# Kernel tuning notes

Measured on AMD Instinct MI355X. Metric: run time of the kernel, lower is better.

Reference implementation:

```python
import jax, jax.numpy as jnp
import numpy as np

DIM = 64
NUM_GRAPHS = 512


def setup_inputs() -> dict:
    key = jax.random.key(0)
    ks = jax.random.split(key, 24)
    N, E, F = 20000, 60000, 11
    rn = lambda k, s, sc: jax.random.normal(k, s, jnp.float32) * sc
    return {
        "x": jax.random.normal(ks[0], (N, F), jnp.float32),
        "edge_index": jax.random.randint(ks[1], (2, E), 0, N),
        "edge_attr": jax.random.uniform(ks[2], (E, 5), jnp.float32),
        "batch": jnp.sort(jax.random.randint(ks[3], (N,), 0, NUM_GRAPHS)),
        # lin0: num_features -> dim
        "lin0_w": rn(ks[4], (DIM, F), 0.3), "lin0_b": jnp.zeros(DIM, jnp.float32),
        # edge MLP: 5 -> 128 -> dim*dim
        "nn1_w": rn(ks[5], (128, 5), 0.3), "nn1_b": jnp.zeros(128, jnp.float32),
        "nn2_w": rn(ks[6], (DIM * DIM, 128), 0.02), "nn2_b": jnp.zeros(DIM * DIM, jnp.float32),
        # NNConv root weight + bias
        "root_w": rn(ks[7], (DIM, DIM), 0.1), "conv_b": jnp.zeros(DIM, jnp.float32),
        # GRU (input dim, hidden dim) gates r,z,n
        "gru_w_ih": rn(ks[8], (3 * DIM, DIM), 0.1), "gru_w_hh": rn(ks[9], (3 * DIM, DIM), 0.1),
        "gru_b_ih": jnp.zeros(3 * DIM, jnp.float32), "gru_b_hh": jnp.zeros(3 * DIM, jnp.float32),
        # Set2Set LSTM: input 2*dim, hidden dim, gates i,f,g,o
        "lstm_w_ih": rn(ks[10], (4 * DIM, 2 * DIM), 0.1), "lstm_w_hh": rn(ks[11], (4 * DIM, DIM), 0.1),
        "lstm_b_ih": jnp.zeros(4 * DIM, jnp.float32), "lstm_b_hh": jnp.zeros(4 * DIM, jnp.float32),
        # readout
        "lin1_w": rn(ks[12], (DIM, 2 * DIM), 0.1), "lin1_b": jnp.zeros(DIM, jnp.float32),
        "lin2_w": rn(ks[13], (1, DIM), 0.1), "lin2_b": jnp.zeros(1, jnp.float32),
    }


def reference(x, edge_index, edge_attr, batch,
              lin0_w, lin0_b, nn1_w, nn1_b, nn2_w, nn2_b, root_w, conv_b,
              gru_w_ih, gru_w_hh, gru_b_ih, gru_b_hh,
              lstm_w_ih, lstm_w_hh, lstm_b_ih, lstm_b_hh,
              lin1_w, lin1_b, lin2_w, lin2_b):
    N = x.shape[0]
    src, dst = edge_index[0], edge_index[1]
    # per-edge weight matrices from edge MLP (edge_attr is constant across the 3 conv calls)
    We = (jax.nn.relu(edge_attr @ nn1_w.T + nn1_b) @ nn2_w.T + nn2_b).reshape(-1, DIM, DIM)
    deg = jnp.maximum(jax.ops.segment_sum(jnp.ones_like(src, jnp.float32), dst, N), 1.0)[:, None]

    out = jax.nn.relu(x @ lin0_w.T + lin0_b)
    h = out  # GRU hidden, shape [N, dim]
    for _ in range(3):
        # NNConv: gather src -> per-edge matmul -> scatter-mean at dst, plus root + bias
        msg = jnp.einsum('ei,eio->eo', out[src], We)
        agg = jax.ops.segment_sum(msg, dst, N) / deg
        m = jax.nn.relu(agg + out @ root_w.T + conv_b)
        # single GRU step (PyTorch gate layout r,z,n)
        gi = m @ gru_w_ih.T + gru_b_ih
        gh = h @ gru_w_hh.T + gru_b_hh
        ir, iz, inn = jnp.split(gi, 3, -1)
        hr, hz, hn = jnp.split(gh, 3, -1)
        r = jax.nn.sigmoid(ir + hr)
        z = jax.nn.sigmoid(iz + hz)
        n = jnp.tanh(inn + r * hn)
        h = (1.0 - z) * n + z * h
        out = h

    # Set2Set pooling, 3 processing steps
    B = NUM_GRAPHS
    q_star = jnp.zeros((B, 2 * DIM), out.dtype)
    hs = jnp.zeros((B, DIM), out.dtype)
    cs = jnp.zeros((B, DIM), out.dtype)
    for _ in range(3):
        gates = q_star @ lstm_w_ih.T + lstm_b_ih + hs @ lstm_w_hh.T + lstm_b_hh
        gi, gf, gg, go = jnp.split(gates, 4, -1)
        cs = jax.nn.sigmoid(gf) * cs + jax.nn.sigmoid(gi) * jnp.tanh(gg)
        hs = jax.nn.sigmoid(go) * jnp.tanh(cs)
        q = hs
        e = jnp.sum(out * q[batch], axis=-1)                 # [N]
        emax = jax.ops.segment_max(e, batch, B)
        a = jnp.exp(e - emax[batch])
        a = a / jax.ops.segment_sum(a, batch, B)[batch]      # scatter-softmax
        r_ = jax.ops.segment_sum(a[:, None] * out, batch, B)  # [B, dim]
        q_star = jnp.concatenate([q, r_], axis=-1)

    y = jax.nn.relu(q_star @ lin1_w.T + lin1_b) @ lin2_w.T + lin2_b
    return y.reshape(-1)
```

## Files before the change

### kernel.cpp

```cpp
#include <hip/hip_runtime.h>
#include <math.h>


typedef _Float16 f16x8 __attribute__((ext_vector_type(8)));
typedef _Float16 h2 __attribute__((ext_vector_type(2)));
typedef float f32x4 __attribute__((ext_vector_type(4)));

#define BFRAG_TOTAL (66 * 4 * 4 * 64 * 8)
#define GFRAG_TOTAL (4 * 16 * 64 * 8)
#define PAIRS_CAP 40064
#define PMAX 152
#define SPLITK 4
#define ITERS 8

#if __has_builtin(__builtin_amdgcn_fdot2)
#define FDOT2(a, b, c) __builtin_amdgcn_fdot2((a), (b), (c), false)
#else
__device__ __forceinline__ float FDOT2(h2 a, h2 b, float c) {
  return c + (float)a[0] * (float)b[0] + (float)a[1] * (float)b[1];
}
#endif

__global__ void k_gptr(const int* __restrict__ batch, int* __restrict__ gptr,
                       int N, int B) {
  int n = blockIdx.x * 256 + threadIdx.x;
  if (n >= N) return;
  int b = batch[n];
  int bp = (n == 0) ? -1 : batch[n - 1];
  for (int g = bp + 1; g <= b; ++g) gptr[g] = n;
  if (n == N - 1) {
    for (int g = b + 1; g <= B; ++g) gptr[g] = N;
  }
}

__global__ void k_cnt(const int* __restrict__ eidx, int* __restrict__ cnt, int E) {
  int e = blockIdx.x * 256 + threadIdx.x;
  if (e < E) atomicAdd(&cnt[eidx[E + e]], 1);
}

__global__ __launch_bounds__(1024) void k_scan(const int* __restrict__ cnt,
                                               int* __restrict__ dptr2, int N) {
  __shared__ int wsum[16];
  int t = threadIdx.x;
  int lane = t & 63, wid = t >> 6;
  if (t == 0) dptr2[0] = 0;
  int running = 0;
  for (int base = 0; base < N; base += 1024) {
    int x = (base + t < N) ? ((cnt[base + t] + 1) & ~1) : 0;
#pragma unroll
    for (int d = 1; d < 64; d <<= 1) {
      int u = __shfl_up(x, d, 64);
      if (lane >= d) x += u;
    }
    if (lane == 63) wsum[wid] = x;
    __syncthreads();
    if (wid == 0) {
      int y = (lane < 16) ? wsum[lane] : 0;
#pragma unroll
      for (int d = 1; d < 16; d <<= 1) {
        int u = __shfl_up(y, d, 64);
        if (lane >= d) y += u;
      }
      if (lane < 16) wsum[lane] = y;
    }
    __syncthreads();
    int add = running + (wid > 0 ? wsum[wid - 1] : 0);
    if (base + t < N) dptr2[base + t + 1] = add + x;
    running += wsum[15];
    __syncthreads();
  }
}

__global__ void k_fill(const int* __restrict__ eidx, const int* __restrict__ dptr2,
                       int* __restrict__ fill, int* __restrict__ srcs_s,
                       int* __restrict__ eord, int E) {
  int e = blockIdx.x * 256 + threadIdx.x;
  if (e >= E) return;
  int d = eidx[E + e];
  int pos = dptr2[d] + atomicAdd(&fill[d], 1);
  srcs_s[pos] = eidx[e];
  eord[pos] = e;
}

__global__ __launch_bounds__(256) void k_h1t(const float* __restrict__ eattr,
                                             const int* __restrict__ eord,
                                             const int* __restrict__ eidx,
                                             const int* __restrict__ cnt,
                                             const float* __restrict__ nn1_w,
                                             const float* __restrict__ nn1_b,
                                             f16x8* __restrict__ hp, int E) {
  __shared__ float w5[640];
  __shared__ float bb[128];
  __shared__ float at[128][10];
  __shared__ float idg[128];
  __shared__ float vf1[128];
  const int t = threadIdx.x;
  const int m0 = blockIdx.x * 128;
  for (int idx = t; idx < 640; idx += 256) w5[idx] = nn1_w[idx];
  if (t < 128) bb[t] = nn1_b[t];
  if (t < 128) {
    int m = m0 + t;
    int e0 = eord[2 * m], e1 = eord[2 * m + 1];
    float iv = 0.f, vf = 0.f;
    if (e0 >= 0) {
      const float* a = eattr + (size_t)e0 * 5;
#pragma unroll
      for (int q = 0; q < 5; ++q) at[t][q] = a[q];
      int dg = cnt[eidx[E + e0]];
      iv = 1.f / (float)(dg > 1 ? dg : 1);
      if (e1 >= 0) {
        const float* b = eattr + (size_t)e1 * 5;
#pragma unroll
        for (int q = 0; q < 5; ++q) at[t][5 + q] = b[q];
        vf = 1.f;
      } else {
#pragma unroll
        for (int q = 0; q < 5; ++q) at[t][5 + q] = 0.f;
      }
    } else {
#pragma unroll
      for (int q = 0; q < 10; ++q) at[t][q] = 0.f;
    }
    idg[t] = iv;
    vf1[t] = vf;
  }
  __syncthreads();
  const int pl = t & 127, jh = (t >> 7) * 64;
  const int m = m0 + pl;
  float a0 = at[pl][0], a1 = at[pl][1], a2 = at[pl][2], a3 = at[pl][3],
        a4 = at[pl][4];
  float b0 = at[pl][5], b1 = at[pl][6], b2 = at[pl][7], b3 = at[pl][8],
        b4 = at[pl][9];
  float iv = idg[pl], vf = vf1[pl];
#pragma unroll 4
  for (int ci = 0; ci < 16; ++ci) {
    int j0 = jh + ci * 4;
    f16x8 o;
#pragma unroll
    for (int u = 0; u < 4; ++u) {
      const float* wr = &w5[(j0 + u) * 5];
      float v0 = fmaxf(bb[j0 + u] + a0 * wr[0] + a1 * wr[1] + a2 * wr[2] +
                           a3 * wr[3] + a4 * wr[4], 0.f) * iv;
      float v1 = fmaxf(bb[j0 + u] + b0 * wr[0] + b1 * wr[1] + b2 * wr[2] +
                           b3 * wr[3] + b4 * wr[4], 0.f) * iv * vf;
      o[2 * u] = (_Float16)v0;
      o[2 * u + 1] = (_Float16)v1;
    }
    hp[(size_t)(j0 >> 2) * PAIRS_CAP + m] = o;
  }
}

__global__ __launch_bounds__(256) void k_bsplit(
    const float* __restrict__ nn2_w, const float* __restrict__ nn2_b,
    const float* __restrict__ root_w, _Float16* __restrict__ Bh,
    _Float16* __restrict__ Bl) {
  __shared__ float lds[4096 * 2];
  const int kc = blockIdx.x;
  const int t = threadIdx.x;
  if (kc < 64) {
    for (int r = t; r < 4096; r += 256) {
      float2 v = *(const float2*)&nn2_w[(size_t)r * 128 + kc * 2];
      lds[r * 2] = v.x;
      lds[r * 2 + 1] = v.y;
    }
  } else if (kc == 64) {
    for (int r = t; r < 4096; r += 256) {
      lds[r * 2] = nn2_b[r];
      lds[r * 2 + 1] = 0.f;
    }
  } else {
    for (int r = t; r < 4096; r += 256) {
      int i = r >> 6, o = r & 63;
      lds[r * 2] = root_w[o * 64 + i];
      lds[r * 2 + 1] = 0.f;
    }
  }
  __syncthreads();
  for (int slot = t; slot < 1024; slot += 256) {
    int lane = slot & 63, c = (slot >> 6) & 3, w = slot >> 8;
    f16x8 ph, pl;
#pragma unroll
    for (int j = 0; j < 8; ++j) {
      int mm = w * 32 + ((lane >> 4) << 3) + j;
      int o = c * 16 + (lane & 15);
      int i = mm & 63, kl = mm >> 6;
      float v = lds[(i * 64 + o) * 2 + kl];
      _Float16 h = (_Float16)v;
      ph[j] = h;
      pl[j] = (_Float16)(v - (float)h);
    }
    size_t base = (((size_t)kc * 4 + w) * 4 + c) * 512 + (size_t)lane * 8;
    *(f16x8*)&Bh[base] = ph;
    *(f16x8*)&Bl[base] = pl;
  }
}

__global__ __launch_bounds__(256) void k_gsplit(
    const float* __restrict__ gw_ih, const float* __restrict__ gw_hh,
    _Float16* __restrict__ Gh, _Float16* __restrict__ Gl) {
  const int c = blockIdx.x;
  const int t = threadIdx.x;
  const int w = t >> 6, lane = t & 63;
  const int part = c >> 2, dblk = c & 3;
  f16x8 oh, ol;
#pragma unroll
  for (int j = 0; j < 8; ++j) {
    int k = w * 32 + ((lane >> 4) << 3) + j;
    int d = dblk * 16 + (lane & 15);
    float v;
    if (part == 0) {
      v = (k < 64) ? gw_ih[(size_t)d * 64 + k] : gw_hh[(size_t)d * 64 + (k - 64)];
    } else if (part == 1) {
      v = (k < 64) ? gw_ih[(size_t)(64 + d) * 64 + k]
                   : gw_hh[(size_t)(64 + d) * 64 + (k - 64)];
    } else if (part == 2) {
      v = (k < 64) ? gw_ih[(size_t)(128 + d) * 64 + k] : 0.f;
    } else {
      v = (k >= 64) ? gw_hh[(size_t)(128 + d) * 64 + (k - 64)] : 0.f;
    }
    _Float16 h = (_Float16)v;
    oh[j] = h;
    ol[j] = (_Float16)(v - (float)h);
  }
  size_t base = ((size_t)(w * 16 + c) * 64 + lane) * 8;
  *(f16x8*)&Gh[base] = oh;
  *(f16x8*)&Gl[base] = ol;
}

__global__ void k_lin0(const float* __restrict__ x, const float* __restrict__ w,
                       const float* __restrict__ b, float* __restrict__ outn, int N) {
  int gid = blockIdx.x * 256 + threadIdx.x;
  int n = gid >> 6, d = gid & 63;
  if (n >= N) return;
  const float* xr = x + (size_t)n * 11;
  const float* wr = w + d * 11;
  float acc = b[d];
#pragma unroll
  for (int f = 0; f < 11; ++f) acc += xr[f] * wr[f];
  outn[(size_t)n * 64 + d] = fmaxf(acc, 0.f);
}

__global__ __launch_bounds__(512, 4) void k_fused(
    const float* __restrict__ outn, const f16x8* __restrict__ hp,
    const int* __restrict__ dptr2, const int* __restrict__ cnt,
    const int* __restrict__ srcs_s, const _Float16* __restrict__ Bh,
    const _Float16* __restrict__ Bl, float* __restrict__ agg2, int N) {
  __shared__ __align__(16) _Float16 Ah[32 * 64 * 8];
  __shared__ uint4 sbufq[PMAX * 17];
  __shared__ uint4 hpq[2][PMAX];

  const int t = threadIdx.x;
  const int w = t >> 6, lane = t & 63;
  const int wq = w & 3;
  const int c_off = (w >> 2) * 2;
  const int nl = t >> 3;
  const int io = t & 7;
  const int split = blockIdx.y;
  const int n0 = blockIdx.x * 64;
  const int n = n0 + nl;
  const bool nvalid = (n < N);
  const int hi_n = (n0 + 64 > N) ? N : (n0 + 64);
  const int p0b = dptr2[n0];
  const int p1b = dptr2[hi_n];
  const int MP0 = p0b >> 1;
  const int MPn = (p1b - p0b) >> 1;
  const bool useLds = (MPn <= PMAX);
  int mp0 = 0, mp1 = 0, deg = 0;
  if (nvalid) { mp0 = dptr2[n] >> 1; mp1 = dptr2[n + 1] >> 1; deg = cnt[n]; }
  const float inv = 1.f / (float)(deg > 1 ? deg : 1);
  const int odd = deg & 1;
  const int rt_b = nl >> 4, nm = nl & 15;
  const int MPs = useLds ? MPn : 0;

  for (int idx = t; idx < MPs * 16; idx += 512) {
    int ml = idx >> 4, g = idx & 15;
    int e0s = srcs_s[2 * (MP0 + ml)];
    int e1s = srcs_s[2 * (MP0 + ml) + 1];
    float4 r0 = *(const float4*)(outn + (size_t)e0s * 64 + g * 4);
    float4 r1 = *(const float4*)(outn + (size_t)e1s * 64 + g * 4);
    f16x8 o;
    o[0] = (_Float16)r0.x; o[1] = (_Float16)r1.x;
    o[2] = (_Float16)r0.y; o[3] = (_Float16)r1.y;
    o[4] = (_Float16)r0.z; o[5] = (_Float16)r1.z;
    o[6] = (_Float16)r0.w; o[7] = (_Float16)r1.w;
    sbufq[ml * 17 + (((g >> 2) ^ (ml & 3)) << 2) + (g & 3)] =
        __builtin_bit_cast(uint4, o);
  }
  for (int idx = t; idx < MPs; idx += 512)
    hpq[0][idx] =
        *(const uint4*)&hp[(size_t)(split * ITERS) * PAIRS_CAP + MP0 + idx];
  __syncthreads();

  f32x4 acc[4][2];
#pragma unroll
  for (int a = 0; a < 4; ++a)
#pragma unroll
    for (int c = 0; c < 2; ++c) acc[a][c] = (f32x4)(0.f);

  const int niter = (split == 0) ? (ITERS + 1) : ITERS;
  int cur = 0;
  for (int cc = 0; cc < niter; ++cc) {
    const bool extra = (cc == ITERS);

    float av[4][8];
#pragma unroll
    for (int kl = 0; kl < 4; ++kl)
#pragma unroll
      for (int j = 0; j < 8; ++j) av[kl][j] = 0.f;

    if (!extra) {
      if (useLds) {
        for (int m = mp0; m < mp1; ++m) {
          int ml = m - MP0;
          uint4 hu = hpq[cur][ml];
          h2 h0 = __builtin_bit_cast(h2, hu.x);
          h2 h1 = __builtin_bit_cast(h2, hu.y);
          h2 hh2 = __builtin_bit_cast(h2, hu.z);
          h2 h3 = __builtin_bit_cast(h2, hu.w);
          int sb = ml * 17 + (((io >> 1) ^ (ml & 3)) << 2) + (io & 1) * 2;
          uint4 su0 = sbufq[sb], su1 = sbufq[sb + 1];
          unsigned vs[8] = {su0.x, su0.y, su0.z, su0.w,
                            su1.x, su1.y, su1.z, su1.w};
#pragma unroll
          for (int v = 0; v < 8; ++v) {
            h2 sp = __builtin_bit_cast(h2, vs[v]);
            av[0][v] = FDOT2(h0, sp, av[0][v]);
            av[1][v] = FDOT2(h1, sp, av[1][v]);
            av[2][v] = FDOT2(hh2, sp, av[2][v]);
            av[3][v] = FDOT2(h3, sp, av[3][v]);
          }
        }
      } else {
        const f16x8* hc = hp + (size_t)(split * ITERS + cc) * PAIRS_CAP;
        for (int m = mp0; m < mp1; ++m) {
          f16x8 hv = hc[m];
          int e0s = srcs_s[2 * m], e1s = srcs_s[2 * m + 1];
          const float4* pa = (const float4*)(outn + (size_t)e0s * 64 + io * 8);
          const float4* pb = (const float4*)(outn + (size_t)e1s * 64 + io * 8);
          float4 a0 = pa[0], a1 = pa[1];
          float4 c0 = pb[0], c1 = pb[1];
          float sv0[8] = {a0.x, a0.y, a0.z, a0.w, a1.x, a1.y, a1.z, a1.w};
          float sv1[8] = {c0.x, c0.y, c0.z, c0.w, c1.x, c1.y, c1.z, c1.w};
#pragma unroll
          for (int kl = 0; kl < 4; ++kl) {
            float hA = (float)hv[2 * kl], hB = (float)hv[2 * kl + 1];
#pragma unroll
            for (int j = 0; j < 8; ++j)
              av[kl][j] += hA * sv0[j] + hB * sv1[j];
          }
        }
      }
    } else {
      if (useLds) {
        for (int m = mp0; m < mp1; ++m) {
          int ml = m - MP0;
          h2 msk;
          msk[0] = (_Float16)1.f;
          msk[1] = (_Float16)((odd && m == mp1 - 1) ? 0.f : 1.f);
          int sb = ml * 17 + (((io >> 1) ^ (ml & 3)) << 2) + (io & 1) * 2;
          uint4 su0 = sbufq[sb], su1 = sbufq[sb + 1];
          unsigned vs[8] = {su0.x, su0.y, su0.z, su0.w,
                            su1.x, su1.y, su1.z, su1.w};
#pragma unroll
          for (int v = 0; v < 8; ++v) {
            h2 sp = __builtin_bit_cast(h2, vs[v]);
            av[0][v] = FDOT2(msk, sp, av[0][v]);
          }
        }
      } else {
        for (int m = mp0; m < mp1; ++m) {
          float m1 = (odd && m == mp1 - 1) ? 0.f : 1.f;
          int e0s = srcs_s[2 * m], e1s = srcs_s[2 * m + 1];
          const float4* pa = (const float4*)(outn + (size_t)e0s * 64 + io * 8);
          const float4* pb = (const float4*)(outn + (size_t)e1s * 64 + io * 8);
          float4 a0 = pa[0], a1 = pa[1];
          float4 c0 = pb[0], c1 = pb[1];
          float sv0[8] = {a0.x, a0.y, a0.z, a0.w, a1.x, a1.y, a1.z, a1.w};
          float sv1[8] = {c0.x, c0.y, c0.z, c0.w, c1.x, c1.y, c1.z, c1.w};
#pragma unroll
          for (int j = 0; j < 8; ++j) av[0][j] += sv0[j] + m1 * sv1[j];
        }
      }
#pragma unroll
      for (int j = 0; j < 8; ++j) av[0][j] *= inv;
      if (nvalid) {
        const float4* sp = (const float4*)(outn + (size_t)n * 64 + io * 8);
        float4 s0 = sp[0], s1 = sp[1];
        float sv[8] = {s0.x, s0.y, s0.z, s0.w, s1.x, s1.y, s1.z, s1.w};
#pragma unroll
        for (int j = 0; j < 8; ++j) av[2][j] = sv[j];
      }
    }

#pragma unroll
    for (int kl = 0; kl < 4; ++kl) {
      const int wb = (kl & 1) * 2 + (io >> 2);
      const int q = ((io >> 1) & 1) * 2 + (io & 1);
      const int fb = (kl >> 1) * 16 + wb * 4 + rt_b;
      const int base = (fb * 64 + (q << 4) + nm) * 8;
      f16x8 phv;
#pragma unroll
      for (int jj = 0; jj < 8; ++jj) phv[jj] = (_Float16)av[kl][jj];
      *(f16x8*)&Ah[base] = phv;
    }
    __syncthreads();

#pragma unroll
    for (int ph = 0; ph < 2; ++ph) {
      const int kco = extra ? (64 + ph) : (split * 16 + cc * 2 + ph);
      f16x8 ah[4];
#pragma unroll
      for (int rt = 0; rt < 4; ++rt)
        ah[rt] = *(const f16x8*)&Ah[((ph * 16 + wq * 4 + rt) * 64 + lane) * 8];
      if (ph == 0 && t < 256 && cc + 1 < ITERS) {
        const uint4* hc =
            (const uint4*)&hp[(size_t)(split * ITERS + cc + 1) * PAIRS_CAP + MP0];
        for (int idx = t; idx < MPs; idx += 256) hpq[cur ^ 1][idx] = hc[idx];
      }
      size_t bbase = ((size_t)(kco * 4 + wq) * 4) * 512;
#pragma unroll
      for (int c2 = 0; c2 < 2; ++c2) {
        const int c = c_off + c2;
        f16x8 bh = *(const f16x8*)&Bh[bbase + c * 512 + lane * 8];
        f16x8 bl = *(const f16x8*)&Bl[bbase + c * 512 + lane * 8];
#pragma unroll
        for (int rt = 0; rt < 4; ++rt) {
          acc[rt][c2] = __builtin_amdgcn_mfma_f32_16x16x32_f16(ah[rt], bh, acc[rt][c2], 0, 0, 0);
          acc[rt][c2] = __builtin_amdgcn_mfma_f32_16x16x32_f16(ah[rt], bl, acc[rt][c2], 0, 0, 0);
        }
      }
    }
    __syncthreads();
    if (cc + 1 < ITERS) cur ^= 1;
  }

  {
    float* redb = (float*)Ah;
    const int qrow = (lane >> 4) * 4, col15 = lane & 15;
    const int g14 = ((lane >> 4) & 1) << 4;
    if (wq == 1 || wq == 3) {
      float* L = redb + (wq >> 1) * 4096;
#pragma unroll
      for (int rt = 0; rt < 4; ++rt)
#pragma unroll
        for (int r = 0; r < 4; ++r) {
          int row = rt * 16 + qrow + r;
#pragma unroll
          for (int c2 = 0; c2 < 2; ++c2) {
            int col = (c_off + c2) * 16 + col15;
            L[row * 64 + (col ^ g14)] = acc[rt][c2][r];
          }
        }
    }
    __syncthreads();
    if (wq == 0 || wq == 2) {
      const float* L = redb + (wq >> 1) * 4096;
#pragma unroll
      for (int rt = 0; rt < 4; ++rt)
#pragma unroll
        for (int r = 0; r < 4; ++r) {
          int row = rt * 16 + qrow + r;
#pragma unroll
          for (int c2 = 0; c2 < 2; ++c2) {
            int col = (c_off + c2) * 16 + col15;
            acc[rt][c2][r] += L[row * 64 + (col ^ g14)];
          }
        }
    }
    __syncthreads();
    if (wq == 2) {
      float* L = redb;
#pragma unroll
      for (int rt = 0; rt < 4; ++rt)
#pragma unroll
        for (int r = 0; r < 4; ++r) {
          int row = rt * 16 + qrow + r;
#pragma unroll
          for (int c2 = 0; c2 < 2; ++c2) {
            int col = (c_off + c2) * 16 + col15;
            L[row * 64 + (col ^ g14)] = acc[rt][c2][r];
          }
        }
    }
    __syncthreads();
    if (wq == 0) {
      const float* L = redb;
      float* ag = agg2 + (size_t)split * (size_t)N * 64;
#pragma unroll
      for (int rt = 0; rt < 4; ++rt)
#pragma unroll
        for (int r = 0; r < 4; ++r) {
          int row = rt * 16 + qrow + r;
          int nn = n0 + row;
          if (nn < N) {
#pragma unroll
            for (int c2 = 0; c2 < 2; ++c2) {
              int col = (c_off + c2) * 16 + col15;
              float v = acc[rt][c2][r] + L[row * 64 + (col ^ g14)];
              ag[(size_t)nn * 64 + col] = v;
            }
          }
        }
    }
  }
}

__global__ __launch_bounds__(512) void k_gru2(
    const float* __restrict__ agg2, const float* __restrict__ conv_b,
    const _Float16* __restrict__ Gh, const _Float16* __restrict__ Gl,
    const float* __restrict__ gb_ih, const float* __restrict__ gb_hh,
    float* __restrict__ outn, int N) {
  __shared__ __align__(16) _Float16 Afrag[16 * 64 * 8];
  __shared__ float bih[192], bhh[192];
  const int t = threadIdx.x;
  const int n0 = blockIdx.x * 64;
  const size_t NN = (size_t)N * 64;
  if (t < 192) { bih[t] = gb_ih[t]; bhh[t] = gb_hh[t]; }

  {
    const int nl = t >> 3, io = t & 7;
    const int n = n0 + nl;
    float v[16];
    if (n < N) {
      if (io < 4) {
        const int d0 = io * 16;
        const size_t base = (size_t)n * 64 + d0;
#pragma unroll
        for (int q = 0; q < 4; ++q) {
          float4 s0 = *(const float4*)&agg2[base + q * 4];
          float4 s1 = *(const float4*)&agg2[NN + base + q * 4];
          float4 s2 = *(const float4*)&agg2[2 * NN + base + q * 4];
          float4 s3 = *(const float4*)&agg2[3 * NN + base + q * 4];
          float4 cb = *(const float4*)&conv_b[d0 + q * 4];
          v[q * 4 + 0] = fmaxf(s0.x + s1.x + s2.x + s3.x + cb.x, 0.f);
          v[q * 4 + 1] = fmaxf(s0.y + s1.y + s2.y + s3.y + cb.y, 0.f);
          v[q * 4 + 2] = fmaxf(s0.z + s1.z + s2.z + s3.z + cb.z, 0.f);
          v[q * 4 + 3] = fmaxf(s0.w + s1.w + s2.w + s3.w + cb.w, 0.f);
        }
      } else {
        const int d0 = (io - 4) * 16;
#pragma unroll
        for (int q = 0; q < 4; ++q) {
          float4 h4 = *(const float4*)&outn[(size_t)n * 64 + d0 + q * 4];
          v[q * 4 + 0] = h4.x;
          v[q * 4 + 1] = h4.y;
          v[q * 4 + 2] = h4.z;
          v[q * 4 + 3] = h4.w;
        }
      }
    } else {
#pragma unroll
      for (int j = 0; j < 16; ++j) v[j] = 0.f;
    }
    const int rt = nl >> 4, m = nl & 15;
#pragma unroll
    for (int g2 = 0; g2 < 2; ++g2) {
      int k0 = io * 16 + g2 * 8;
      int ksub = k0 >> 5, kgrp = (k0 >> 3) & 3;
      f16x8 o;
#pragma unroll
      for (int jj = 0; jj < 8; ++jj) o[jj] = (_Float16)v[g2 * 8 + jj];
      *(f16x8*)&Afrag[((ksub * 4 + rt) * 64 + (kgrp << 4) + m) * 8] = o;
    }
  }
  __syncthreads();

  const int w = t >> 6, lane = t & 63;
  const int rt = w >> 1, q2 = (w & 1) * 2;
  f32x4 acc[8];
#pragma unroll
  for (int i = 0; i < 8; ++i) acc[i] = (f32x4)(0.f);
#pragma unroll
  for (int ks = 0; ks < 4; ++ks) {
    f16x8 ah = *(const f16x8*)&Afrag[((ks * 4 + rt) * 64 + lane) * 8];
#pragma unroll
    for (int idx = 0; idx < 8; ++idx) {
      int c = (idx >> 1) * 4 + q2 + (idx & 1);
      f16x8 gh = *(const f16x8*)&Gh[((size_t)(ks * 16 + c) * 64 + lane) * 8];
      f16x8 gl = *(const f16x8*)&Gl[((size_t)(ks * 16 + c) * 64 + lane) * 8];
      acc[idx] = __builtin_amdgcn_mfma_f32_16x16x32_f16(ah, gh, acc[idx], 0, 0, 0);
      acc[idx] = __builtin_amdgcn_mfma_f32_16x16x32_f16(ah, gl, acc[idx], 0, 0, 0);
    }
  }
  const int qrow = (lane >> 4) * 4, col = lane & 15;
#pragma unroll
  for (int c01 = 0; c01 < 2; ++c01) {
    const int d = (q2 + c01) * 16 + col;
#pragma unroll
    for (int r = 0; r < 4; ++r) {
      const int n = n0 + rt * 16 + qrow + r;
      if (n < N) {
        float rs = acc[c01][r], zs = acc[2 + c01][r];
        float inn = acc[4 + c01][r], hn = acc[6 + c01][r];
        float h = outn[(size_t)n * 64 + d];
        float rg = 1.f / (1.f + expf(-(rs + bih[d] + bhh[d])));
        float zg = 1.f / (1.f + expf(-(zs + bih[64 + d] + bhh[64 + d])));
        float ng = tanhf(inn + bih[128 + d] + rg * (hn + bhh[128 + d]));
        outn[(size_t)n * 64 + d] = (1.f - zg) * ng + zg * h;
      }
    }
  }
}

__global__ __launch_bounds__(256) void k_s2s(
    const float* __restrict__ outn, const int* __restrict__ gptr,
    const float* __restrict__ w_ih, const float* __restrict__ w_hh,
    const float* __restrict__ b_ih, const float* __restrict__ b_hh,
    const float* __restrict__ w1, const float* __restrict__ b1,
    const float* __restrict__ w2, const float* __restrict__ b2,
    float* __restrict__ y) {
  __shared__ float q[128];
  __shared__ float hsL[64];
  __shared__ float csL[64];
  __shared__ float gate[256];
  __shared__ float red[4][66];
  const int b = blockIdx.x, t = threadIdx.x;
  const int wv = t >> 6, d = t & 63;
  const int n0 = gptr[b], n1 = gptr[b + 1];
  if (t < 128) q[t] = 0.f;
  if (t < 64) { hsL[t] = 0.f; csL[t] = 0.f; }
  __syncthreads();

  for (int step = 0; step < 3; ++step) {
    float acc = b_ih[t] + b_hh[t];
    const float* wi = w_ih + t * 128;
    const float* wh = w_hh + t * 64;
#pragma unroll 4
    for (int k = 0; k < 128; ++k) acc += wi[k] * q[k];
#pragma unroll 4
    for (int k = 0; k < 64; ++k) acc += wh[k] * hsL[k];
    gate[t] = acc;
    __syncthreads();
    if (t < 64) {
      float ig = gate[t], fg = gate[64 + t], gg = gate[128 + t],
            og = gate[192 + t];
      float c = csL[t];
      float si = 1.f / (1.f + expf(-ig));
      float sf = 1.f / (1.f + expf(-fg));
      float so = 1.f / (1.f + expf(-og));
      float cn = sf * c + si * tanhf(gg);
      csL[t] = cn;
      hsL[t] = so * tanhf(cn);
    }
    __syncthreads();

    float qd = hsL[d];
    float mx = -3.4e38f, den = 0.f, racc = 0.f;
    for (int nn = n0 + wv; nn < n1; nn += 4) {
      float od = outn[(size_t)nn * 64 + d];
      float v = od * qd;
      for (int s = 32; s > 0; s >>= 1) v += __shfl_xor(v, s);
      float mnew = fmaxf(mx, v);
      float scale = expf(mx - mnew);
      float a = expf(v - mnew);
      den = den * scale + a;
      racc = racc * scale + a * od;
      mx = mnew;
    }
    if (d == 0) { red[wv][0] = mx; red[wv][1] = den; }
    red[wv][2 + d] = racc;
    __syncthreads();
    if (t < 64) {
      float M = fmaxf(fmaxf(red[0][0], red[1][0]), fmaxf(red[2][0], red[3][0]));
      float dd = 0.f, rr = 0.f;
#pragma unroll
      for (int ww = 0; ww < 4; ++ww) {
        float sc = expf(red[ww][0] - M);
        dd += red[ww][1] * sc;
        rr += red[ww][2 + t] * sc;
      }
      float r = (dd > 0.f) ? rr / dd : 0.f;
      q[t] = hsL[t];
      q[64 + t] = r;
    }
    __syncthreads();
  }

  if (t < 64) {
    float acc = b1[t];
    const float* wr = w1 + t * 128;
#pragma unroll 4
    for (int k = 0; k < 128; ++k) acc += wr[k] * q[k];
    acc = fmaxf(acc, 0.f) * w2[t];
    for (int s = 32; s > 0; s >>= 1) acc += __shfl_xor(acc, s);
    if (t == 0) y[b] = acc + b2[0];
  }
}

extern "C" void kernel_launch(void* const* d_in, const int* in_sizes, int n_in,
                              void* d_out, int out_size, void* d_ws,
                              size_t ws_size, hipStream_t stream) {
  (void)n_in; (void)out_size; (void)ws_size;
  const float* x      = (const float*)d_in[0];
  const int*   eidx   = (const int*)d_in[1];
  const float* eattr  = (const float*)d_in[2];
  const int*   batch  = (const int*)d_in[3];
  const float* lin0_w = (const float*)d_in[4];
  const float* lin0_b = (const float*)d_in[5];
  const float* nn1_w  = (const float*)d_in[6];
  const float* nn1_b  = (const float*)d_in[7];
  const float* nn2_w  = (const float*)d_in[8];
  const float* nn2_b  = (const float*)d_in[9];
  const float* root_w = (const float*)d_in[10];
  const float* conv_b = (const float*)d_in[11];
  const float* gw_ih  = (const float*)d_in[12];
  const float* gw_hh  = (const float*)d_in[13];
  const float* gb_ih  = (const float*)d_in[14];
  const float* gb_hh  = (const float*)d_in[15];
  const float* lw_ih  = (const float*)d_in[16];
  const float* lw_hh  = (const float*)d_in[17];
  const float* lb_ih  = (const float*)d_in[18];
  const float* lb_hh  = (const float*)d_in[19];
  const float* lin1_w = (const float*)d_in[20];
  const float* lin1_b = (const float*)d_in[21];
  const float* lin2_w = (const float*)d_in[22];
  const float* lin2_b = (const float*)d_in[23];

  const int N = in_sizes[0] / 11;
  const int E = in_sizes[1] / 2;
  const int B = 512;

  size_t off = 0;
  auto bump = [&](size_t bytes) {
    size_t o = off;
    off += (bytes + 255) & ~(size_t)255;
    return o;
  };
  char* base = (char*)d_ws;
  float*     outn   = (float*)(base + bump((size_t)N * 64 * 4));
  float*     agg2   = (float*)(base + bump((size_t)SPLITK * N * 64 * 4));
  f16x8*     hpG    = (f16x8*)(base + bump((size_t)32 * PAIRS_CAP * 16));
  _Float16*  Bh     = (_Float16*)(base + bump((size_t)BFRAG_TOTAL * 2));
  _Float16*  Bl     = (_Float16*)(base + bump((size_t)BFRAG_TOTAL * 2));
  _Float16*  Gh     = (_Float16*)(base + bump((size_t)GFRAG_TOTAL * 2));
  _Float16*  Gl     = (_Float16*)(base + bump((size_t)GFRAG_TOTAL * 2));
  int*       cnt    = (int*)(base + bump((size_t)2 * N * 4));
  int*       fill   = cnt + N;
  int*       dptr2  = (int*)(base + bump((size_t)(N + 1) * 4));
  int*       srcs_s = (int*)(base + bump((size_t)2 * PAIRS_CAP * 4));
  int*       eord   = (int*)(base + bump((size_t)2 * PAIRS_CAP * 4));
  int*       gptr   = (int*)(base + bump((size_t)(B + 1) * 4));

  hipMemsetAsync(cnt, 0, (size_t)2 * N * 4, stream);
  hipMemsetAsync(srcs_s, 0, (size_t)2 * PAIRS_CAP * 4, stream);
  hipMemsetAsync(eord, 0xFF, (size_t)2 * PAIRS_CAP * 4, stream);

  k_gptr<<<(N + 255) / 256, 256, 0, stream>>>(batch, gptr, N, B);
  k_cnt<<<(E + 255) / 256, 256, 0, stream>>>(eidx, cnt, E);
  k_scan<<<1, 1024, 0, stream>>>(cnt, dptr2, N);
  k_fill<<<(E + 255) / 256, 256, 0, stream>>>(eidx, dptr2, fill, srcs_s, eord, E);
  k_h1t<<<PAIRS_CAP / 128, 256, 0, stream>>>(eattr, eord, eidx, cnt, nn1_w,
                                             nn1_b, hpG, E);
  k_bsplit<<<66, 256, 0, stream>>>(nn2_w, nn2_b, root_w, Bh, Bl);
  k_gsplit<<<16, 256, 0, stream>>>(gw_ih, gw_hh, Gh, Gl);
  k_lin0<<<(N * 64 + 255) / 256, 256, 0, stream>>>(x, lin0_w, lin0_b, outn, N);

  const int NBLK = (N + 63) / 64;
  for (int it = 0; it < 3; ++it) {
    k_fused<<<dim3(NBLK, SPLITK), 512, 0, stream>>>(outn, hpG, dptr2, cnt,
                                                    srcs_s, Bh, Bl, agg2, N);
    k_gru2<<<NBLK, 512, 0, stream>>>(agg2, conv_b, Gh, Gl, gb_ih, gb_hh, outn,
                                     N);
  }

  k_s2s<<<B, 256, 0, stream>>>(outn, gptr, lw_ih, lw_hh, lb_ih, lb_hh, lin1_w,
                               lin1_b, lin2_w, lin2_b, (float*)d_out);
}
```

Before: 628.8 us.

## Process two hidden-chunk slices per gather pass in fused NNConv kernel

Halves the number of outer iterations per split by computing eight h-chunk dot products per edge pair instead of four. Each loaded source-feature pair from LDS is reused for twice as many FDOT2s, cutting the repeated LDS reads and loop overhead. The MFMA stage then runs twice per iteration over the doubled accumulators. The cost is doubled av register pressure (64 floats), which at launch_bounds(512,4) may cause spills, and the hp prefetch now lands between the two sub-passes.

```diff
diff --git a/kernel.cpp b/kernel.cpp
--- a/kernel.cpp
+++ b/kernel.cpp
@@ -11,7 +11,7 @@
 #define PAIRS_CAP 40064
 #define PMAX 152
 #define SPLITK 4
-#define ITERS 8
+#define ITERS 4
 
 #if __has_builtin(__builtin_amdgcn_fdot2)
 #define FDOT2(a, b, c) __builtin_amdgcn_fdot2((a), (b), (c), false)
@@ -247,7 +247,7 @@
     const _Float16* __restrict__ Bl, float* __restrict__ agg2, int N) {
   __shared__ __align__(16) _Float16 Ah[32 * 64 * 8];
   __shared__ uint4 sbufq[PMAX * 17];
-  __shared__ uint4 hpq[2][PMAX];
+  __shared__ uint4 hpq[2 * PMAX];
 
   const int t = threadIdx.x;
   const int w = t >> 6, lane = t & 63;
@@ -286,9 +286,12 @@
     sbufq[ml * 17 + (((g >> 2) ^ (ml & 3)) << 2) + (g & 3)] =
         __builtin_bit_cast(uint4, o);
   }
-  for (int idx = t; idx < MPs; idx += 512)
-    hpq[0][idx] =
-        *(const uint4*)&hp[(size_t)(split * ITERS) * PAIRS_CAP + MP0 + idx];
+  for (int idx = t; idx < MPs; idx += 512) {
+    hpq[idx] =
+        *(const uint4*)&hp[(size_t)(split * 8) * PAIRS_CAP + MP0 + idx];
+    hpq[PMAX + idx] =
+        *(const uint4*)&hp[(size_t)(split * 8 + 1) * PAIRS_CAP + MP0 + idx];
+  }
   __syncthreads();
 
   f32x4 acc[4][2];
@@ -298,13 +301,12 @@
     for (int c = 0; c < 2; ++c) acc[a][c] = (f32x4)(0.f);
 
   const int niter = (split == 0) ? (ITERS + 1) : ITERS;
-  int cur = 0;
   for (int cc = 0; cc < niter; ++cc) {
     const bool extra = (cc == ITERS);
 
-    float av[4][8];
-#pragma unroll
-    for (int kl = 0; kl < 4; ++kl)
+    float av[8][8];
+#pragma unroll
+    for (int kl = 0; kl < 8; ++kl)
 #pragma unroll
       for (int j = 0; j < 8; ++j) av[kl][j] = 0.f;
 
@@ -312,11 +314,16 @@
       if (useLds) {
         for (int m = mp0; m < mp1; ++m) {
           int ml = m - MP0;
-          uint4 hu = hpq[cur][ml];
-          h2 h0 = __builtin_bit_cast(h2, hu.x);
-          h2 h1 = __builtin_bit_cast(h2, hu.y);
-          h2 hh2 = __builtin_bit_cast(h2, hu.z);
-          h2 h3 = __builtin_bit_cast(h2, hu.w);
+          uint4 hu0 = hpq[ml];
+          uint4 hu1 = hpq[PMAX + ml];
+          h2 hh0 = __builtin_bit_cast(h2, hu0.x);
+          h2 hh1 = __builtin_bit_cast(h2, hu0.y);
+          h2 hh2 = __builtin_bit_cast(h2, hu0.z);
+          h2 hh3 = __builtin_bit_cast(h2, hu0.w);
+          h2 hh4 = __builtin_bit_cast(h2, hu1.x);
+          h2 hh5 = __builtin_bit_cast(h2, hu1.y);
+          h2 hh6 = __builtin_bit_cast(h2, hu1.z);
+          h2 hh7 = __builtin_bit_cast(h2, hu1.w);
           int sb = ml * 17 + (((io >> 1) ^ (ml & 3)) << 2) + (io & 1) * 2;
           uint4 su0 = sbufq[sb], su1 = sbufq[sb + 1];
           unsigned vs[8] = {su0.x, su0.y, su0.z, su0.w,
@@ -324,16 +331,22 @@
 #pragma unroll
           for (int v = 0; v < 8; ++v) {
             h2 sp = __builtin_bit_cast(h2, vs[v]);
-            av[0][v] = FDOT2(h0, sp, av[0][v]);
-            av[1][v] = FDOT2(h1, sp, av[1][v]);
+            av[0][v] = FDOT2(hh0, sp, av[0][v]);
+            av[1][v] = FDOT2(hh1, sp, av[1][v]);
             av[2][v] = FDOT2(hh2, sp, av[2][v]);
-            av[3][v] = FDOT2(h3, sp, av[3][v]);
+            av[3][v] = FDOT2(hh3, sp, av[3][v]);
+            av[4][v] = FDOT2(hh4, sp, av[4][v]);
+            av[5][v] = FDOT2(hh5, sp, av[5][v]);
+            av[6][v] = FDOT2(hh6, sp, av[6][v]);
+            av[7][v] = FDOT2(hh7, sp, av[7][v]);
           }
         }
       } else {
-        const f16x8* hc = hp + (size_t)(split * ITERS + cc) * PAIRS_CAP;
+        const f16x8* hcA = hp + (size_t)(split * 8 + 2 * cc) * PAIRS_CAP;
+        const f16x8* hcB = hp + (size_t)(split * 8 + 2 * cc + 1) * PAIRS_CAP;
         for (int m = mp0; m < mp1; ++m) {
-          f16x8 hv = hc[m];
+          f16x8 hv0 = hcA[m];
+          f16x8 hv1 = hcB[m];
           int e0s = srcs_s[2 * m], e1s = srcs_s[2 * m + 1];
           const float4* pa = (const float4*)(outn + (size_t)e0s * 64 + io * 8);
           const float4* pb = (const float4*)(outn + (size_t)e1s * 64 + io * 8);
@@ -343,10 +356,13 @@
           float sv1[8] = {c0.x, c0.y, c0.z, c0.w, c1.x, c1.y, c1.z, c1.w};
 #pragma unroll
           for (int kl = 0; kl < 4; ++kl) {
-            float hA = (float)hv[2 * kl], hB = (float)hv[2 * kl + 1];
-#pragma unroll
-            for (int j = 0; j < 8; ++j)
-              av[kl][j] += hA * sv0[j] + hB * sv1[j];
+            float hA0 = (float)hv0[2 * kl], hB0 = (float)hv0[2 * kl + 1];
+            float hA1 = (float)hv1[2 * kl], hB1 = (float)hv1[2 * kl + 1];
+#pragma unroll
+            for (int j = 0; j < 8; ++j) {
+              av[kl][j] += hA0 * sv0[j] + hB0 * sv1[j];
+              av[4 + kl][j] += hA1 * sv0[j] + hB1 * sv1[j];
+            }
           }
         }
       }
@@ -392,46 +408,54 @@
       }
     }
 
-#pragma unroll
-    for (int kl = 0; kl < 4; ++kl) {
-      const int wb = (kl & 1) * 2 + (io >> 2);
-      const int q = ((io >> 1) & 1) * 2 + (io & 1);
-      const int fb = (kl >> 1) * 16 + wb * 4 + rt_b;
-      const int base = (fb * 64 + (q << 4) + nm) * 8;
-      f16x8 phv;
-#pragma unroll
-      for (int jj = 0; jj < 8; ++jj) phv[jj] = (_Float16)av[kl][jj];
-      *(f16x8*)&Ah[base] = phv;
-    }
-    __syncthreads();
-
-#pragma unroll
-    for (int ph = 0; ph < 2; ++ph) {
-      const int kco = extra ? (64 + ph) : (split * 16 + cc * 2 + ph);
-      f16x8 ah[4];
-#pragma unroll
-      for (int rt = 0; rt < 4; ++rt)
-        ah[rt] = *(const f16x8*)&Ah[((ph * 16 + wq * 4 + rt) * 64 + lane) * 8];
-      if (ph == 0 && t < 256 && cc + 1 < ITERS) {
-        const uint4* hc =
-            (const uint4*)&hp[(size_t)(split * ITERS + cc + 1) * PAIRS_CAP + MP0];
-        for (int idx = t; idx < MPs; idx += 256) hpq[cur ^ 1][idx] = hc[idx];
-      }
-      size_t bbase = ((size_t)(kco * 4 + wq) * 4) * 512;
-#pragma unroll
-      for (int c2 = 0; c2 < 2; ++c2) {
-        const int c = c_off + c2;
-        f16x8 bh = *(const f16x8*)&Bh[bbase + c * 512 + lane * 8];
-        f16x8 bl = *(const f16x8*)&Bl[bbase + c * 512 + lane * 8];
-#pragma unroll
-        for (int rt = 0; rt < 4; ++rt) {
-          acc[rt][c2] = __builtin_amdgcn_mfma_f32_16x16x32_f16(ah[rt], bh, acc[rt][c2], 0, 0, 0);
-          acc[rt][c2] = __builtin_amdgcn_mfma_f32_16x16x32_f16(ah[rt], bl, acc[rt][c2], 0, 0, 0);
-        }
-      }
-    }
-    __syncthreads();
-    if (cc + 1 < ITERS) cur ^= 1;
+    const int pmax = extra ? 1 : 2;
+    for (int p = 0; p < pmax; ++p) {
+#pragma unroll
+      for (int kll = 0; kll < 4; ++kll) {
+        const float* avp = av[p * 4 + kll];
+        const int wb = (kll & 1) * 2 + (io >> 2);
+        const int q = ((io >> 1) & 1) * 2 + (io & 1);
+        const int fb = (kll >> 1) * 16 + wb * 4 + rt_b;
+        const int base = (fb * 64 + (q << 4) + nm) * 8;
+        f16x8 phv;
+#pragma unroll
+        for (int jj = 0; jj < 8; ++jj) phv[jj] = (_Float16)avp[jj];
+        *(f16x8*)&Ah[base] = phv;
+      }
+      __syncthreads();
+
+#pragma unroll
+      for (int ph = 0; ph < 2; ++ph) {
+        const int kco = extra ? (64 + ph) : (split * 16 + cc * 4 + p * 2 + ph);
+        f16x8 ah[4];
+#pragma unroll
+        for (int rt = 0; rt < 4; ++rt)
+          ah[rt] = *(const f16x8*)&Ah[((ph * 16 + wq * 4 + rt) * 64 + lane) * 8];
+        if (p == 0 && ph == 0 && cc + 1 < ITERS) {
+          const uint4* hcA =
+              (const uint4*)&hp[(size_t)(split * 8 + 2 * (cc + 1)) * PAIRS_CAP + MP0];
+          const uint4* hcB =
+              (const uint4*)&hp[(size_t)(split * 8 + 2 * (cc + 1) + 1) * PAIRS_CAP + MP0];
+          for (int idx = t; idx < MPs; idx += 512) {
+            hpq[idx] = hcA[idx];
+            hpq[PMAX + idx] = hcB[idx];
+          }
+        }
+        size_t bbase = ((size_t)(kco * 4 + wq) * 4) * 512;
+#pragma unroll
+        for (int c2 = 0; c2 < 2; ++c2) {
+          const int c = c_off + c2;
+          f16x8 bh = *(const f16x8*)&Bh[bbase + c * 512 + lane * 8];
+          f16x8 bl = *(const f16x8*)&Bl[bbase + c * 512 + lane * 8];
+#pragma unroll
+          for (int rt = 0; rt < 4; ++rt) {
+            acc[rt][c2] = __builtin_amdgcn_mfma_f32_16x16x32_f16(ah[rt], bh, acc[rt][c2], 0, 0, 0);
+            acc[rt][c2] = __builtin_amdgcn_mfma_f32_16x16x32_f16(ah[rt], bl, acc[rt][c2], 0, 0, 0);
+          }
+        }
+      }
+      __syncthreads();
+    }
   }
 
   {
```

Measured after the change: 1.293 ms. 106% more time.
